# Kernel optimization log

Hardware: AMD Instinct MI355X
Metric: run time of the kernel (lower is better)

Reference implementation:

```python
import jax, jax.numpy as jnp
import numpy as np

H, W, F = 64, 64, 64  # ca_shape and inner_filters
N = H * W  # flattened attention length

def conv2d_same(x, Wt, b):
    # x: [B,H,W,Cin], Wt: [kh,kw,Cin,Cout] (HWIO)
    y = jax.lax.conv_general_dilated(x, Wt, window_strides=(1, 1), padding='SAME',
                                     dimension_numbers=('NHWC', 'HWIO', 'NHWC'))
    return y + b

def setup_inputs() -> dict:
    key = jax.random.key(0)
    ks = jax.random.split(key, 9)
    s = 0.05  # small init scale to keep softmax logits sane
    return {
        'x':  jax.random.normal(ks[0], (4, H, W, 64), jnp.float32),
        'Wk': jax.random.normal(ks[1], (3, 3, 64, F), jnp.float32) * s,
        'bk': jnp.zeros((F,), jnp.float32),
        'Wq': jax.random.normal(ks[2], (3, 3, 64, F), jnp.float32) * s,
        'bq': jnp.zeros((F,), jnp.float32),
        'Wv': jax.random.normal(ks[3], (3, 3, 64, F), jnp.float32) * s,
        'bv': jnp.zeros((F,), jnp.float32),
        'Wr': jax.random.normal(ks[4], (3, 3, F, 64), jnp.float32) * s,
        'br': jnp.zeros((64,), jnp.float32),
    }

def reference(x, Wk, bk, Wq, bq, Wv, bv, Wr, br):
    B = x.shape[0]
    k = jax.nn.elu(conv2d_same(x, Wk, bk)).reshape(B, N, F)
    q = jax.nn.elu(conv2d_same(x, Wq, bq)).reshape(B, N, F)
    v = jax.nn.relu(conv2d_same(x, Wv, bv)).reshape(B, N, F)
    # QK^T with diagonal zeroed (multiplied by 1 - I, NOT -inf), then scaled
    scores = jnp.einsum('bnf,bmf->bnm', q, k)
    mask = 1.0 - jnp.eye(N, dtype=scores.dtype)  # broadcast over batch
    scores = scores * mask / jnp.sqrt(jnp.asarray(F, scores.dtype))
    attn = jax.nn.softmax(scores, axis=-1)
    out = jnp.einsum('bnm,bmf->bnf', attn, v).reshape(B, H, W, F)
    return jax.nn.relu(conv2d_same(out, Wr, br))
```

## Files before the change

### kernel.cpp

```cpp
#include <hip/hip_runtime.h>
#include <hip/hip_bf16.h>
#include <math.h>

#define B_ 4
#define H_ 64
#define W_ 64
#define C_ 64
#define F_ 64
#define N_ 4096

typedef __attribute__((ext_vector_type(8))) short bf16x8;
typedef __attribute__((ext_vector_type(4))) short bf16x4;
typedef __attribute__((ext_vector_type(4))) float f32x4;

static __device__ __forceinline__ short f2bf(float f){
  union { __hip_bfloat16 h; short s; } u;
  u.h = __float2bfloat16(f);
  return u.s;
}

__global__ __launch_bounds__(256) void prep_x_kernel(
    const float* __restrict__ x, short* __restrict__ xb)
{
  const int i4 = blockIdx.x * 256 + threadIdx.x;
  const float4 v = ((const float4*)x)[i4];
  bf16x4 o;
  o[0] = f2bf(v.x); o[1] = f2bf(v.y); o[2] = f2bf(v.z); o[3] = f2bf(v.w);
  ((bf16x4*)xb)[i4] = o;
}

__global__ __launch_bounds__(256) void prep_w_kernel(
    const float* __restrict__ Wk, const float* __restrict__ Wq,
    const float* __restrict__ Wv, const float* __restrict__ Wr,
    short* __restrict__ Wt)
{
  const int gid = blockIdx.x * 256 + threadIdx.x;
  const int oc = gid / 576;
  const int kk = gid % 576;
  const int srcofs = (kk >> 6) * 4096 + (kk & 63) * 64 + (oc & 63);
  const float* src = (oc < 64) ? Wk : (oc < 128) ? Wq : (oc < 192) ? Wv : Wr;
  Wt[gid] = f2bf(src[srcofs]);
}

__global__ __launch_bounds__(256) void conv_qkv_mfma(
    const short* __restrict__ xb, const short* __restrict__ Wt,
    const float* __restrict__ bk, const float* __restrict__ bq,
    const float* __restrict__ bv,
    short* __restrict__ qo, short* __restrict__ ko, short* __restrict__ vt)
{
  const int lane = threadIdx.x & 63;
  const int w    = threadIdx.x >> 6;
  const int lrow = lane & 15;
  const int lkb  = lane >> 4;
  const int p0   = blockIdx.x << 5;
  const int b    = p0 >> 12;
  const int y    = (p0 >> 6) & 63;
  const int x0   = p0 & 63;

  f32x4 ak[2], aq[2], av[2];
  #pragma unroll
  for (int m = 0; m < 2; ++m)
    #pragma unroll
    for (int i = 0; i < 4; ++i){ ak[m][i] = 0.f; aq[m][i] = 0.f; av[m][i] = 0.f; }

  const short* wr_k = Wt + (      w * 16 + lrow) * 576;
  const short* wr_q = Wt + ( 64 + w * 16 + lrow) * 576;
  const short* wr_v = Wt + (128 + w * 16 + lrow) * 576;

  #pragma unroll
  for (int ks = 0; ks < 18; ++ks){
    const int kxy = ks >> 1;
    const int ky  = kxy / 3;
    const int kx  = kxy - ky * 3;
    const int ci0 = (ks & 1) << 5;
    const int yy  = y + ky - 1;
    const bf16x8 wk8 = *(const bf16x8*)(wr_k + ks * 32 + lkb * 8);
    const bf16x8 wq8 = *(const bf16x8*)(wr_q + ks * 32 + lkb * 8);
    const bf16x8 wv8 = *(const bf16x8*)(wr_v + ks * 32 + lkb * 8);
    #pragma unroll
    for (int m = 0; m < 2; ++m){
      const int xx = x0 + m * 16 + lrow + kx - 1;
      bf16x8 a = {0,0,0,0,0,0,0,0};
      if ((unsigned)yy < 64u && (unsigned)xx < 64u)
        a = *(const bf16x8*)(xb + ((((b << 6) + yy) << 6) + xx) * 64 + ci0 + lkb * 8);
      ak[m] = __builtin_amdgcn_mfma_f32_16x16x32_bf16(a, wk8, ak[m], 0, 0, 0);
      aq[m] = __builtin_amdgcn_mfma_f32_16x16x32_bf16(a, wq8, aq[m], 0, 0, 0);
      av[m] = __builtin_amdgcn_mfma_f32_16x16x32_bf16(a, wv8, av[m], 0, 0, 0);
    }
  }
  const int oc = w * 16 + lrow;
  const float bkv = bk[oc], bqv = bq[oc], bvv = bv[oc];
  #pragma unroll
  for (int m = 0; m < 2; ++m){
    bf16x4 vp;
    #pragma unroll
    for (int i = 0; i < 4; ++i){
      const int p = p0 + m * 16 + (lkb << 2) + i;
      const float kvv = ak[m][i] + bkv;
      ko[p * 64 + oc] = f2bf(kvv > 0.f ? kvv : expm1f(kvv));
      const float qvv = aq[m][i] + bqv;
      const float qe  = (qvv > 0.f ? qvv : expm1f(qvv)) * 0.125f;
      qo[p * 64 + oc] = f2bf(qe);
      const float vvv = av[m][i] + bvv;
      vp[i] = f2bf(vvv > 0.f ? vvv : 0.f);
    }
    *(bf16x4*)(vt + ((size_t)(b * 64 + oc)) * 4096 + (p0 & 4095) + m * 16 + (lkb << 2)) = vp;
  }
}

__global__ __launch_bounds__(256, 3) void attn_kernel(
    const short* __restrict__ q, const short* __restrict__ k,
    const short* __restrict__ vt, float* __restrict__ Op,
    float* __restrict__ lp, int split)
{
  const int tid  = threadIdx.x;
  const int lane = tid & 63;
  const int wv   = tid >> 6;
  const int lrow = lane & 15;
  const int lkb  = lane >> 4;

  const int bid  = blockIdx.x;
  const int b    = bid / (32 * split);
  const int rem  = bid % (32 * split);
  const int rt   = rem / split;
  const int sp   = rem % split;
  const int rbase = (rt << 7) + (wv << 5);
  const int tiles = (N_ / 64) / split;
  const int ct0   = sp * tiles;

  const short* qb = q  + (size_t)b * N_ * F_;
  const short* kb = k  + (size_t)b * N_ * F_;
  const short* vb = vt + (size_t)b * F_ * N_;

  const bf16x8 aq00 = *(const bf16x8*)(qb + (rbase +      lrow) * F_ + lkb * 8);
  const bf16x8 aq01 = *(const bf16x8*)(qb + (rbase +      lrow) * F_ + 32 + lkb * 8);
  const bf16x8 aq10 = *(const bf16x8*)(qb + (rbase + 16 + lrow) * F_ + lkb * 8);
  const bf16x8 aq11 = *(const bf16x8*)(qb + (rbase + 16 + lrow) * F_ + 32 + lkb * 8);

  __shared__ short kbuf[2][64 * 64];
  __shared__ short vbuf[2][64 * 64];
  __shared__ short p_lds[4][2][16][72];

  const int srow = tid >> 3;
  const int sc16 = tid & 7;
  const int dst0 = (srow * 128)        + ((sc16 * 16) ^ ((srow & 7) << 4));
  const int dst1 = ((srow + 32) * 128) + ((sc16 * 16) ^ ((srow & 7) << 4));

  float l_r[2][4];
  f32x4 oacc[2][4];
  #pragma unroll
  for (int g = 0; g < 2; ++g){
    #pragma unroll
    for (int i = 0; i < 4; ++i) l_r[g][i] = 0.f;
    #pragma unroll
    for (int fs = 0; fs < 4; ++fs)
      #pragma unroll
      for (int i = 0; i < 4; ++i) oacc[g][fs][i] = 0.f;
  }

  int cbase = ct0 << 6;
  bf16x8 sk0 = *(const bf16x8*)(kb + (cbase + srow) * 64      + sc16 * 8);
  bf16x8 sk1 = *(const bf16x8*)(kb + (cbase + srow + 32) * 64 + sc16 * 8);
  bf16x8 sv0 = *(const bf16x8*)(vb + (size_t)srow * N_        + cbase + sc16 * 8);
  bf16x8 sv1 = *(const bf16x8*)(vb + (size_t)(srow + 32) * N_ + cbase + sc16 * 8);
  *(bf16x8*)((char*)kbuf[0] + dst0) = sk0;
  *(bf16x8*)((char*)kbuf[0] + dst1) = sk1;
  *(bf16x8*)((char*)vbuf[0] + dst0) = sv0;
  *(bf16x8*)((char*)vbuf[0] + dst1) = sv1;
  __syncthreads();

  int cur = 0;
  for (int t = 0; t < tiles; ++t){
    cbase = (ct0 + t) << 6;
    if (t + 1 < tiles){
      const int cb2 = (ct0 + t + 1) << 6;
      sk0 = *(const bf16x8*)(kb + (cb2 + srow) * 64      + sc16 * 8);
      sk1 = *(const bf16x8*)(kb + (cb2 + srow + 32) * 64 + sc16 * 8);
      sv0 = *(const bf16x8*)(vb + (size_t)srow * N_        + cb2 + sc16 * 8);
      sv1 = *(const bf16x8*)(vb + (size_t)(srow + 32) * N_ + cb2 + sc16 * 8);
    }
    const char* kc = (const char*)kbuf[cur];
    const char* vc = (const char*)vbuf[cur];
    f32x4 s0[4], s1[4];
    #pragma unroll
    for (int n = 0; n < 4; ++n){
      #pragma unroll
      for (int i = 0; i < 4; ++i){ s0[n][i] = 0.f; s1[n][i] = 0.f; }
    }
    #pragma unroll
    for (int n = 0; n < 4; ++n){
      const int r   = n * 16 + lrow;
      const int swz = (r & 7) << 4;
      const bf16x8 b0 = *(const bf16x8*)(kc + r * 128 + ((lkb * 16) ^ swz));
      const bf16x8 b1 = *(const bf16x8*)(kc + r * 128 + ((64 + lkb * 16) ^ swz));
      s0[n] = __builtin_amdgcn_mfma_f32_16x16x32_bf16(aq00, b0, s0[n], 0, 0, 0);
      s0[n] = __builtin_amdgcn_mfma_f32_16x16x32_bf16(aq01, b1, s0[n], 0, 0, 0);
      s1[n] = __builtin_amdgcn_mfma_f32_16x16x32_bf16(aq10, b0, s1[n], 0, 0, 0);
      s1[n] = __builtin_amdgcn_mfma_f32_16x16x32_bf16(aq11, b1, s1[n], 0, 0, 0);
    }
    #pragma unroll
    for (int g = 0; g < 2; ++g){
      f32x4* s = g ? s1 : s0;
      const int rb = rbase + g * 16 + lkb * 4;
      #pragma unroll
      for (int n = 0; n < 4; ++n){
        const int gc = cbase + n * 16 + lrow;
        #pragma unroll
        for (int i = 0; i < 4; ++i){
          float sv = s[n][i];
          if (rb + i == gc) sv = 0.f;
          const float p = exp2f(fmaf(sv, 1.44269504f, -23.0831206f));
          l_r[g][i] += p;
          p_lds[wv][g][lkb * 4 + i][n * 16 + lrow] = f2bf(p);
        }
      }
    }
    #pragma unroll
    for (int kc2 = 0; kc2 < 2; ++kc2){
      const bf16x8 pa0 = *(const bf16x8*)(&p_lds[wv][0][lrow][kc2 * 32 + lkb * 8]);
      const bf16x8 pa1 = *(const bf16x8*)(&p_lds[wv][1][lrow][kc2 * 32 + lkb * 8]);
      #pragma unroll
      for (int fs = 0; fs < 4; ++fs){
        const int r   = fs * 16 + lrow;
        const int swz = (r & 7) << 4;
        const bf16x8 bvf = *(const bf16x8*)(vc + r * 128 + ((kc2 * 64 + lkb * 16) ^ swz));
        oacc[0][fs] = __builtin_amdgcn_mfma_f32_16x16x32_bf16(pa0, bvf, oacc[0][fs], 0, 0, 0);
        oacc[1][fs] = __builtin_amdgcn_mfma_f32_16x16x32_bf16(pa1, bvf, oacc[1][fs], 0, 0, 0);
      }
    }
    __syncthreads();
    if (t + 1 < tiles){
      const int nxt = cur ^ 1;
      *(bf16x8*)((char*)kbuf[nxt] + dst0) = sk0;
      *(bf16x8*)((char*)kbuf[nxt] + dst1) = sk1;
      *(bf16x8*)((char*)vbuf[nxt] + dst0) = sv0;
      *(bf16x8*)((char*)vbuf[nxt] + dst1) = sv1;
    }
    __syncthreads();
    cur ^= 1;
  }
  float* Ob = Op + (size_t)(b * split + sp) * N_ * F_;
  #pragma unroll
  for (int g = 0; g < 2; ++g){
    #pragma unroll
    for (int i = 0; i < 4; ++i){
      #pragma unroll
      for (int d = 1; d < 16; d <<= 1)
        l_r[g][i] += __shfl_xor(l_r[g][i], d, 64);
      const int row = rbase + g * 16 + lkb * 4 + i;
      #pragma unroll
      for (int fs = 0; fs < 4; ++fs)
        Ob[(size_t)row * F_ + fs * 16 + lrow] = oacc[g][fs][i];
      if (lrow == 0)
        lp[(size_t)(b * split + sp) * N_ + row] = l_r[g][i];
    }
  }
}

__global__ __launch_bounds__(256) void combine_kernel(
    const float* __restrict__ Op, const float* __restrict__ lp,
    short* __restrict__ ob, int split)
{
  const int gid = blockIdx.x * 256 + threadIdx.x;
  const int f = gid & 63;
  const int n = (gid >> 6) & (N_ - 1);
  const int b = gid >> 18;
  float L = 0.f, O = 0.f;
  for (int s = 0; s < split; ++s){
    L += lp[(size_t)(b * split + s) * N_ + n];
    O += Op[((size_t)(b * split + s) * N_ + n) * F_ + f];
  }
  ob[gid] = f2bf(O / L);
}

__global__ __launch_bounds__(256) void conv_out_mfma(
    const short* __restrict__ ab, const short* __restrict__ Wt,
    const float* __restrict__ br, float* __restrict__ out)
{
  const int lane = threadIdx.x & 63;
  const int w    = threadIdx.x >> 6;
  const int lrow = lane & 15;
  const int lkb  = lane >> 4;
  const int p0   = blockIdx.x << 5;
  const int b    = p0 >> 12;
  const int y    = (p0 >> 6) & 63;
  const int x0   = p0 & 63;

  f32x4 acc[2];
  #pragma unroll
  for (int m = 0; m < 2; ++m)
    #pragma unroll
    for (int i = 0; i < 4; ++i) acc[m][i] = 0.f;
  const short* wr = Wt + (192 + w * 16 + lrow) * 576;

  #pragma unroll
  for (int ks = 0; ks < 18; ++ks){
    const int kxy = ks >> 1;
    const int ky  = kxy / 3;
    const int kx  = kxy - ky * 3;
    const int ci0 = (ks & 1) << 5;
    const int yy  = y + ky - 1;
    const bf16x8 w8 = *(const bf16x8*)(wr + ks * 32 + lkb * 8);
    #pragma unroll
    for (int m = 0; m < 2; ++m){
      const int xx = x0 + m * 16 + lrow + kx - 1;
      bf16x8 a = {0,0,0,0,0,0,0,0};
      if ((unsigned)yy < 64u && (unsigned)xx < 64u)
        a = *(const bf16x8*)(ab + ((((b << 6) + yy) << 6) + xx) * 64 + ci0 + lkb * 8);
      acc[m] = __builtin_amdgcn_mfma_f32_16x16x32_bf16(a, w8, acc[m], 0, 0, 0);
    }
  }
  const int oc = w * 16 + lrow;
  const float bb = br[oc];
  #pragma unroll
  for (int m = 0; m < 2; ++m)
    #pragma unroll
    for (int i = 0; i < 4; ++i){
      const int p = p0 + m * 16 + (lkb << 2) + i;
      out[(size_t)p * 64 + oc] = fmaxf(acc[m][i] + bb, 0.f);
    }
}

extern "C" void kernel_launch(void* const* d_in, const int* in_sizes, int n_in,
                              void* d_out, int out_size, void* d_ws, size_t ws_size,
                              hipStream_t stream)
{
  const float* x  = (const float*)d_in[0];
  const float* Wk = (const float*)d_in[1];
  const float* bk = (const float*)d_in[2];
  const float* Wq = (const float*)d_in[3];
  const float* bq = (const float*)d_in[4];
  const float* Wv = (const float*)d_in[5];
  const float* bv = (const float*)d_in[6];
  const float* Wr = (const float*)d_in[7];
  const float* br = (const float*)d_in[8];
  float* out = (float*)d_out;

  const size_t BNF = (size_t)B_ * N_ * F_;
  const size_t fixed_shorts = BNF * 5 + 256 * 576;
  const size_t fixed_bytes  = fixed_shorts * 2;
  int split = 8;
  while (split > 1 &&
         fixed_bytes + (size_t)split * (BNF * 4 + (size_t)B_ * N_ * 4) > ws_size)
    split >>= 1;

  short* xb16 = (short*)d_ws;
  short* Wt   = xb16 + BNF;
  short* qw   = Wt + 256 * 576;
  short* kw   = qw + BNF;
  short* vt   = kw + BNF;
  short* attnb= vt + BNF;
  float* Op   = (float*)(attnb + BNF);
  float* lp   = Op + (size_t)split * BNF;

  hipLaunchKernelGGL(prep_x_kernel, dim3(1024), dim3(256), 0, stream, x, xb16);
  hipLaunchKernelGGL(prep_w_kernel, dim3(576), dim3(256), 0, stream, Wk, Wq, Wv, Wr, Wt);
  hipLaunchKernelGGL(conv_qkv_mfma, dim3(512), dim3(256), 0, stream,
                     xb16, Wt, bk, bq, bv, qw, kw, vt);
  hipLaunchKernelGGL(attn_kernel, dim3(B_ * 32 * split), dim3(256), 0, stream,
                     qw, kw, vt, Op, lp, split);
  hipLaunchKernelGGL(combine_kernel, dim3((B_ * N_ * F_) / 256), dim3(256), 0, stream,
                     Op, lp, attnb, split);
  hipLaunchKernelGGL(conv_out_mfma, dim3(512), dim3(256), 0, stream,
                     attnb, Wt, br, out);
}
```

Measured before the change: 99.40 us.

## Compute softmax row sums via MFMA, store bf16 partials, drop a barrier

The attention kernel now accumulates the softmax denominators with an MFMA against a ones vector, replacing per-element scalar adds and the final shuffle reduction. The probability tile per wave shrinks to one swizzled 16x64 buffer reused per row group, and the diagonal mask is applied only on tiles that contain the diagonal. Exp uses __expf with a truncating bf16 conversion, one __syncthreads per iteration is removed, and split partial outputs are written as bf16 instead of fp32, halving combine traffic. Occupancy hint rises to 4 blocks per CU. These add rounding error to both the partials and the row sums and rely on the per-wave LDS buffer being safe without the removed barrier.

```diff
diff --git a/kernel.cpp b/kernel.cpp
--- a/kernel.cpp
+++ b/kernel.cpp
@@ -17,6 +17,11 @@
   union { __hip_bfloat16 h; short s; } u;
   u.h = __float2bfloat16(f);
   return u.s;
+}
+static __device__ __forceinline__ float bf2f(short s){
+  union { unsigned u; float f; } v;
+  v.u = ((unsigned)(unsigned short)s) << 16;
+  return v.f;
 }
 
 __global__ __launch_bounds__(256) void prep_x_kernel(
@@ -108,9 +113,9 @@
   }
 }
 
-__global__ __launch_bounds__(256, 3) void attn_kernel(
+__global__ __launch_bounds__(256, 4) void attn_kernel(
     const short* __restrict__ q, const short* __restrict__ k,
-    const short* __restrict__ vt, float* __restrict__ Op,
+    const short* __restrict__ vt, short* __restrict__ Opb,
     float* __restrict__ lp, int split)
 {
   const int tid  = threadIdx.x;
@@ -139,19 +144,23 @@
 
   __shared__ short kbuf[2][64 * 64];
   __shared__ short vbuf[2][64 * 64];
-  __shared__ short p_lds[4][2][16][72];
+  __shared__ short p_lds[4][16][64];
+
+  bf16x8 ones;
+  #pragma unroll
+  for (int j = 0; j < 8; ++j) ones[j] = (short)0x3F80;
 
   const int srow = tid >> 3;
   const int sc16 = tid & 7;
   const int dst0 = (srow * 128)        + ((sc16 * 16) ^ ((srow & 7) << 4));
   const int dst1 = ((srow + 32) * 128) + ((sc16 * 16) ^ ((srow & 7) << 4));
 
-  float l_r[2][4];
   f32x4 oacc[2][4];
+  f32x4 lacc[2];
   #pragma unroll
   for (int g = 0; g < 2; ++g){
     #pragma unroll
-    for (int i = 0; i < 4; ++i) l_r[g][i] = 0.f;
+    for (int i = 0; i < 4; ++i) lacc[g][i] = 0.f;
     #pragma unroll
     for (int fs = 0; fs < 4; ++fs)
       #pragma unroll
@@ -198,37 +207,44 @@
       s1[n] = __builtin_amdgcn_mfma_f32_16x16x32_bf16(aq10, b0, s1[n], 0, 0, 0);
       s1[n] = __builtin_amdgcn_mfma_f32_16x16x32_bf16(aq11, b1, s1[n], 0, 0, 0);
     }
+    char* pb = (char*)p_lds + wv * 2048;
+    const int rswz = (lrow & 7) << 4;
     #pragma unroll
     for (int g = 0; g < 2; ++g){
       f32x4* s = g ? s1 : s0;
-      const int rb = rbase + g * 16 + lkb * 4;
+      if (((rbase + g * 16) >> 6) == (ct0 + t)){
+        const int dn = (wv * 2 + g) & 3;
+        #pragma unroll
+        for (int i = 0; i < 4; ++i)
+          if (lrow == lkb * 4 + i) s[dn][i] = 0.f;
+      }
       #pragma unroll
       for (int n = 0; n < 4; ++n){
-        const int gc = cbase + n * 16 + lrow;
         #pragma unroll
         for (int i = 0; i < 4; ++i){
-          float sv = s[n][i];
-          if (rb + i == gc) sv = 0.f;
-          const float p = exp2f(fmaf(sv, 1.44269504f, -23.0831206f));
-          l_r[g][i] += p;
-          p_lds[wv][g][lkb * 4 + i][n * 16 + lrow] = f2bf(p);
+          union { float f; unsigned u; } cv;
+          cv.f = __expf(s[n][i] - 16.f);
+          const int row = lkb * 4 + i;
+          *(short*)(pb + row * 128 + (((n * 16 + lrow) * 2) ^ ((row & 7) << 4))) =
+              (short)(cv.u >> 16);
         }
       }
-    }
-    #pragma unroll
-    for (int kc2 = 0; kc2 < 2; ++kc2){
-      const bf16x8 pa0 = *(const bf16x8*)(&p_lds[wv][0][lrow][kc2 * 32 + lkb * 8]);
-      const bf16x8 pa1 = *(const bf16x8*)(&p_lds[wv][1][lrow][kc2 * 32 + lkb * 8]);
-      #pragma unroll
-      for (int fs = 0; fs < 4; ++fs){
-        const int r   = fs * 16 + lrow;
-        const int swz = (r & 7) << 4;
-        const bf16x8 bvf = *(const bf16x8*)(vc + r * 128 + ((kc2 * 64 + lkb * 16) ^ swz));
-        oacc[0][fs] = __builtin_amdgcn_mfma_f32_16x16x32_bf16(pa0, bvf, oacc[0][fs], 0, 0, 0);
-        oacc[1][fs] = __builtin_amdgcn_mfma_f32_16x16x32_bf16(pa1, bvf, oacc[1][fs], 0, 0, 0);
+      const bf16x8 pa0 = *(const bf16x8*)(pb + lrow * 128 + ((lkb * 16) ^ rswz));
+      const bf16x8 pa1 = *(const bf16x8*)(pb + lrow * 128 + ((64 + lkb * 16) ^ rswz));
+      lacc[g] = __builtin_amdgcn_mfma_f32_16x16x32_bf16(pa0, ones, lacc[g], 0, 0, 0);
+      lacc[g] = __builtin_amdgcn_mfma_f32_16x16x32_bf16(pa1, ones, lacc[g], 0, 0, 0);
+      #pragma unroll
+      for (int kc2 = 0; kc2 < 2; ++kc2){
+        const bf16x8 pa = kc2 ? pa1 : pa0;
+        #pragma unroll
+        for (int fs = 0; fs < 4; ++fs){
+          const int r   = fs * 16 + lrow;
+          const int swz = (r & 7) << 4;
+          const bf16x8 bvf = *(const bf16x8*)(vc + r * 128 + ((kc2 * 64 + lkb * 16) ^ swz));
+          oacc[g][fs] = __builtin_amdgcn_mfma_f32_16x16x32_bf16(pa, bvf, oacc[g][fs], 0, 0, 0);
+        }
       }
     }
-    __syncthreads();
     if (t + 1 < tiles){
       const int nxt = cur ^ 1;
       *(bf16x8*)((char*)kbuf[nxt] + dst0) = sk0;
@@ -239,26 +255,23 @@
     __syncthreads();
     cur ^= 1;
   }
-  float* Ob = Op + (size_t)(b * split + sp) * N_ * F_;
+  short* Ob = Opb + (size_t)(b * split + sp) * N_ * F_;
   #pragma unroll
   for (int g = 0; g < 2; ++g){
     #pragma unroll
     for (int i = 0; i < 4; ++i){
-      #pragma unroll
-      for (int d = 1; d < 16; d <<= 1)
-        l_r[g][i] += __shfl_xor(l_r[g][i], d, 64);
       const int row = rbase + g * 16 + lkb * 4 + i;
       #pragma unroll
       for (int fs = 0; fs < 4; ++fs)
-        Ob[(size_t)row * F_ + fs * 16 + lrow] = oacc[g][fs][i];
+        Ob[(size_t)row * F_ + fs * 16 + lrow] = f2bf(oacc[g][fs][i]);
       if (lrow == 0)
-        lp[(size_t)(b * split + sp) * N_ + row] = l_r[g][i];
+        lp[(size_t)(b * split + sp) * N_ + row] = lacc[g][i];
     }
   }
 }
 
 __global__ __launch_bounds__(256) void combine_kernel(
-    const float* __restrict__ Op, const float* __restrict__ lp,
+    const short* __restrict__ Opb, const float* __restrict__ lp,
     short* __restrict__ ob, int split)
 {
   const int gid = blockIdx.x * 256 + threadIdx.x;
@@ -268,7 +281,7 @@
   float L = 0.f, O = 0.f;
   for (int s = 0; s < split; ++s){
     L += lp[(size_t)(b * split + s) * N_ + n];
-    O += Op[((size_t)(b * split + s) * N_ + n) * F_ + f];
+    O += bf2f(Opb[((size_t)(b * split + s) * N_ + n) * F_ + f]);
   }
   ob[gid] = f2bf(O / L);
 }
@@ -341,7 +354,7 @@
   const size_t fixed_bytes  = fixed_shorts * 2;
   int split = 8;
   while (split > 1 &&
-         fixed_bytes + (size_t)split * (BNF * 4 + (size_t)B_ * N_ * 4) > ws_size)
+         fixed_bytes + (size_t)split * (BNF * 2 + (size_t)B_ * N_ * 4) > ws_size)
     split >>= 1;
 
   short* xb16 = (short*)d_ws;
@@ -350,17 +363,17 @@
   short* kw   = qw + BNF;
   short* vt   = kw + BNF;
   short* attnb= vt + BNF;
-  float* Op   = (float*)(attnb + BNF);
-  float* lp   = Op + (size_t)split * BNF;
+  short* Opb  = attnb + BNF;
+  float* lp   = (float*)(Opb + (size_t)split * BNF);
 
   hipLaunchKernelGGL(prep_x_kernel, dim3(1024), dim3(256), 0, stream, x, xb16);
   hipLaunchKernelGGL(prep_w_kernel, dim3(576), dim3(256), 0, stream, Wk, Wq, Wv, Wr, Wt);
   hipLaunchKernelGGL(conv_qkv_mfma, dim3(512), dim3(256), 0, stream,
                      xb16, Wt, bk, bq, bv, qw, kw, vt);
   hipLaunchKernelGGL(attn_kernel, dim3(B_ * 32 * split), dim3(256), 0, stream,
-                     qw, kw, vt, Op, lp, split);
+                     qw, kw, vt, Opb, lp, split);
   hipLaunchKernelGGL(combine_kernel, dim3((B_ * N_ * F_) / 256), dim3(256), 0, stream,
-                     Op, lp, attnb, split);
+                     Opb, lp, attnb, split);
   hipLaunchKernelGGL(conv_out_mfma, dim3(512), dim3(256), 0, stream,
                      attnb, Wt, br, out);
 }
```

Result: slower. 114.0 us (+14.7%).

## Transpose score MFMA layout to pack P writes and drop a barrier

Applied to the files above, without the earlier changes.

The QK^T MFMA operands are swapped so each lane holds four consecutive key columns of a single query row. Probabilities can then be packed into 8-byte swizzled LDS stores by truncating to bf16, and row sums stay per lane until a final two-step shuffle. The diagonal mask becomes a tile-level check instead of a per-element compare, exp uses __expf, PV is issued per row-group right after its P tile, and one __syncthreads per tile is removed. Truncating instead of rounding to bf16 slightly changes numerics.

```diff
diff --git a/kernel.cpp b/kernel.cpp
--- a/kernel.cpp
+++ b/kernel.cpp
@@ -12,6 +12,7 @@
 typedef __attribute__((ext_vector_type(8))) short bf16x8;
 typedef __attribute__((ext_vector_type(4))) short bf16x4;
 typedef __attribute__((ext_vector_type(4))) float f32x4;
+typedef __attribute__((ext_vector_type(2))) int i32x2;
 
 static __device__ __forceinline__ short f2bf(float f){
   union { __hip_bfloat16 h; short s; } u;
@@ -139,24 +140,21 @@
 
   __shared__ short kbuf[2][64 * 64];
   __shared__ short vbuf[2][64 * 64];
-  __shared__ short p_lds[4][2][16][72];
+  __shared__ short pbuf[4][2][16][64];
 
   const int srow = tid >> 3;
   const int sc16 = tid & 7;
   const int dst0 = (srow * 128)        + ((sc16 * 16) ^ ((srow & 7) << 4));
   const int dst1 = ((srow + 32) * 128) + ((sc16 * 16) ^ ((srow & 7) << 4));
 
-  float l_r[2][4];
   f32x4 oacc[2][4];
-  #pragma unroll
-  for (int g = 0; g < 2; ++g){
-    #pragma unroll
-    for (int i = 0; i < 4; ++i) l_r[g][i] = 0.f;
+  float l_r[2] = {0.f, 0.f};
+  #pragma unroll
+  for (int g = 0; g < 2; ++g)
     #pragma unroll
     for (int fs = 0; fs < 4; ++fs)
       #pragma unroll
       for (int i = 0; i < 4; ++i) oacc[g][fs][i] = 0.f;
-  }
 
   int cbase = ct0 << 6;
   bf16x8 sk0 = *(const bf16x8*)(kb + (cbase + srow) * 64      + sc16 * 8);
@@ -193,42 +191,54 @@
       const int swz = (r & 7) << 4;
       const bf16x8 b0 = *(const bf16x8*)(kc + r * 128 + ((lkb * 16) ^ swz));
       const bf16x8 b1 = *(const bf16x8*)(kc + r * 128 + ((64 + lkb * 16) ^ swz));
-      s0[n] = __builtin_amdgcn_mfma_f32_16x16x32_bf16(aq00, b0, s0[n], 0, 0, 0);
-      s0[n] = __builtin_amdgcn_mfma_f32_16x16x32_bf16(aq01, b1, s0[n], 0, 0, 0);
-      s1[n] = __builtin_amdgcn_mfma_f32_16x16x32_bf16(aq10, b0, s1[n], 0, 0, 0);
-      s1[n] = __builtin_amdgcn_mfma_f32_16x16x32_bf16(aq11, b1, s1[n], 0, 0, 0);
-    }
+      s0[n] = __builtin_amdgcn_mfma_f32_16x16x32_bf16(b0, aq00, s0[n], 0, 0, 0);
+      s0[n] = __builtin_amdgcn_mfma_f32_16x16x32_bf16(b1, aq01, s0[n], 0, 0, 0);
+      s1[n] = __builtin_amdgcn_mfma_f32_16x16x32_bf16(b0, aq10, s1[n], 0, 0, 0);
+      s1[n] = __builtin_amdgcn_mfma_f32_16x16x32_bf16(b1, aq11, s1[n], 0, 0, 0);
+    }
+    const int rswz = (lrow & 7) << 4;
     #pragma unroll
     for (int g = 0; g < 2; ++g){
       f32x4* s = g ? s1 : s0;
-      const int rb = rbase + g * 16 + lkb * 4;
+      const int dq = rbase + g * 16 - cbase;
+      if (dq >= 0 && dq < 64){
+        #pragma unroll
+        for (int n = 0; n < 4; ++n)
+          if (dq == n * 16){
+            const int di = lrow - (lkb << 2);
+            #pragma unroll
+            for (int i = 0; i < 4; ++i)
+              if (di == i) s[n][i] = 0.f;
+          }
+      }
+      char* pgc = (char*)&pbuf[wv][g][0][0];
       #pragma unroll
       for (int n = 0; n < 4; ++n){
-        const int gc = cbase + n * 16 + lrow;
+        union { float f; unsigned u; } c0, c1, c2, c3;
+        c0.f = __expf(s[n][0] - 16.f);
+        c1.f = __expf(s[n][1] - 16.f);
+        c2.f = __expf(s[n][2] - 16.f);
+        c3.f = __expf(s[n][3] - 16.f);
+        l_r[g] += (c0.f + c1.f) + (c2.f + c3.f);
+        i32x2 pk;
+        pk[0] = (int)((c1.u & 0xFFFF0000u) | (c0.u >> 16));
+        pk[1] = (int)((c3.u & 0xFFFF0000u) | (c2.u >> 16));
+        *(i32x2*)(pgc + lrow * 128 + ((n * 32 + lkb * 8) ^ rswz)) = pk;
+      }
+      const bf16x8 pa0 = *(const bf16x8*)(pgc + lrow * 128 + ((lkb * 16) ^ rswz));
+      const bf16x8 pa1 = *(const bf16x8*)(pgc + lrow * 128 + ((64 + lkb * 16) ^ rswz));
+      #pragma unroll
+      for (int kc2 = 0; kc2 < 2; ++kc2){
+        const bf16x8 pa = kc2 ? pa1 : pa0;
         #pragma unroll
-        for (int i = 0; i < 4; ++i){
-          float sv = s[n][i];
-          if (rb + i == gc) sv = 0.f;
-          const float p = exp2f(fmaf(sv, 1.44269504f, -23.0831206f));
-          l_r[g][i] += p;
-          p_lds[wv][g][lkb * 4 + i][n * 16 + lrow] = f2bf(p);
+        for (int fs = 0; fs < 4; ++fs){
+          const int r   = fs * 16 + lrow;
+          const int swz = (r & 7) << 4;
+          const bf16x8 bvf = *(const bf16x8*)(vc + r * 128 + ((kc2 * 64 + lkb * 16) ^ swz));
+          oacc[g][fs] = __builtin_amdgcn_mfma_f32_16x16x32_bf16(pa, bvf, oacc[g][fs], 0, 0, 0);
         }
       }
     }
-    #pragma unroll
-    for (int kc2 = 0; kc2 < 2; ++kc2){
-      const bf16x8 pa0 = *(const bf16x8*)(&p_lds[wv][0][lrow][kc2 * 32 + lkb * 8]);
-      const bf16x8 pa1 = *(const bf16x8*)(&p_lds[wv][1][lrow][kc2 * 32 + lkb * 8]);
-      #pragma unroll
-      for (int fs = 0; fs < 4; ++fs){
-        const int r   = fs * 16 + lrow;
-        const int swz = (r & 7) << 4;
-        const bf16x8 bvf = *(const bf16x8*)(vc + r * 128 + ((kc2 * 64 + lkb * 16) ^ swz));
-        oacc[0][fs] = __builtin_amdgcn_mfma_f32_16x16x32_bf16(pa0, bvf, oacc[0][fs], 0, 0, 0);
-        oacc[1][fs] = __builtin_amdgcn_mfma_f32_16x16x32_bf16(pa1, bvf, oacc[1][fs], 0, 0, 0);
-      }
-    }
-    __syncthreads();
     if (t + 1 < tiles){
       const int nxt = cur ^ 1;
       *(bf16x8*)((char*)kbuf[nxt] + dst0) = sk0;
@@ -239,21 +249,23 @@
     __syncthreads();
     cur ^= 1;
   }
+  #pragma unroll
+  for (int g = 0; g < 2; ++g){
+    l_r[g] += __shfl_xor(l_r[g], 16, 64);
+    l_r[g] += __shfl_xor(l_r[g], 32, 64);
+  }
   float* Ob = Op + (size_t)(b * split + sp) * N_ * F_;
   #pragma unroll
   for (int g = 0; g < 2; ++g){
     #pragma unroll
     for (int i = 0; i < 4; ++i){
-      #pragma unroll
-      for (int d = 1; d < 16; d <<= 1)
-        l_r[g][i] += __shfl_xor(l_r[g][i], d, 64);
       const int row = rbase + g * 16 + lkb * 4 + i;
       #pragma unroll
       for (int fs = 0; fs < 4; ++fs)
         Ob[(size_t)row * F_ + fs * 16 + lrow] = oacc[g][fs][i];
-      if (lrow == 0)
-        lp[(size_t)(b * split + sp) * N_ + row] = l_r[g][i];
-    }
+    }
+    if (lane < 16)
+      lp[(size_t)(b * split + sp) * N_ + rbase + g * 16 + lane] = l_r[g];
   }
 }
 
```

After: 91.39 us. -8.1%, faster.
